# Kernel tuning notes

Hardware: AMD Instinct MI355X
Metric: run time of the kernel (lower is better)

## Reference

```python
import jax, jax.numpy as jnp
import numpy as np

N, NODE_F, EDGE_F = 50000, 192, 64
M = 800000  # directed edges
D = NODE_F + EDGE_F  # inner_dim = 256
OUT = 2048
DEPTH = 3


def setup_inputs() -> dict:
    key = jax.random.key(0)
    ks = jax.random.split(key, 8)
    node_attr = jax.random.normal(ks[0], (N, NODE_F), dtype=jnp.float32)
    edge_attr = jax.random.normal(ks[1], (M, EDGE_F), dtype=jnp.float32)
    edge_src = jax.random.randint(ks[2], (M,), 0, N, dtype=jnp.int32)
    edge_dst = jax.random.randint(ks[3], (M,), 0, N, dtype=jnp.int32)
    # per-depth parameters (original stacks copies along a depth axis)
    W_inner = jnp.stack([jnp.eye(D, dtype=jnp.float32)
                         + 0.01 * jax.random.normal(jax.random.fold_in(ks[4], d), (D, D))
                         for d in range(DEPTH)])                      # [DEPTH, D, D]
    b_inner = jnp.zeros((DEPTH, D), dtype=jnp.float32)
    scale = jnp.sqrt(6.0 / (D + OUT)).astype(jnp.float32)            # glorot_uniform
    W_output = jax.random.uniform(ks[5], (DEPTH + 1, D, OUT), jnp.float32, -scale, scale)
    b_output = jnp.zeros((DEPTH + 1, OUT), dtype=jnp.float32)
    return {"node_attr": node_attr, "edge_attr": edge_attr,
            "edge_src": edge_src, "edge_dst": edge_dst,
            "W_inner": W_inner, "b_inner": b_inner,
            "W_output": W_output, "b_output": b_output}


def _fp_contribution(attr, W_out_d, b_out_d):
    # softmax over fingerprint dim per node, summed over nodes -> [OUT]
    return jax.nn.softmax(attr @ W_out_d + b_out_d, axis=-1).sum(axis=0)


def reference(node_attr, edge_attr, edge_src, edge_dst,
              W_inner, b_inner, W_output, b_output):
    n = node_attr.shape[0]
    # attributes = [nodeAttributes | zeros(edge_feat)]  -> [N, D]
    attr = jnp.concatenate(
        [node_attr, jnp.zeros((n, edge_attr.shape[1]), node_attr.dtype)], axis=1)
    fp = _fp_contribution(attr, W_output[0], b_output[0])
    # per-edge payload: [zeros(node_feat) | edgeAttr]  -> [M, D]
    edge_pad = jnp.concatenate(
        [jnp.zeros((edge_attr.shape[0], node_attr.shape[1]), edge_attr.dtype), edge_attr],
        axis=1)
    for d in range(1, DEPTH + 1):
        # v_i = attr_i + sum_{(ni,ei) in nbrs(i)} (attr_ni + [0|edgeAttr_ei])
        msgs = attr[edge_src] + edge_pad                 # [M, D] gather
        agg = jax.ops.segment_sum(msgs, edge_dst, num_segments=n)
        v = attr + agg
        # activation_inner = 'linear' (identity)
        attr = v @ W_inner[d - 1] + b_inner[d - 1]
        fp = fp + _fp_contribution(attr, W_output[d], b_output[d])
    return fp  # [OUT]
```

## Files before the change

### kernel.cpp

```cpp
#include <hip/hip_runtime.h>
#include <hip/hip_bf16.h>

#define N_NODES 50000
#define N_PAD   50016
#define NODE_F  192
#define EDGE_F  64
#define DIM     256
#define OUT_DIM 2048
#define DEPTH   3
#define M_EDGES 800000

typedef short  bf16x8 __attribute__((ext_vector_type(8)));
typedef float  f32x4  __attribute__((ext_vector_type(4)));

__device__ inline short f2bf(float f) {
    unsigned u = __float_as_uint(f);
    unsigned r = (u + 0x7fffu + ((u >> 16) & 1u)) >> 16;
    return (short)r;
}

__global__ void k_init_attr(const float* __restrict__ node_attr,
                            float* __restrict__ attr,
                            short* __restrict__ attr_bf) {
    int i = blockIdx.x * 256 + threadIdx.x;
    int row = i >> 6, q = i & 63;
    if (row >= N_PAD) return;
    float4 v = make_float4(0.f, 0.f, 0.f, 0.f);
    if (row < N_NODES && q < NODE_F / 4)
        v = ((const float4*)node_attr)[row * (NODE_F / 4) + q];
    if (row < N_NODES) ((float4*)attr)[i] = v;
    short4 s; s.x = f2bf(v.x); s.y = f2bf(v.y); s.z = f2bf(v.z); s.w = f2bf(v.w);
    ((short4*)attr_bf)[i] = s;
}

__global__ void k_degree(const int* __restrict__ dst, int* __restrict__ deg) {
    int e = blockIdx.x * 256 + threadIdx.x;
    if (e < M_EDGES) atomicAdd(&deg[dst[e]], 1);
}

__global__ __launch_bounds__(1024) void k_scan(int* __restrict__ deg,
                                               int* __restrict__ rowptr) {
    __shared__ int part[1024];
    int t = threadIdx.x;
    const int CH = (N_NODES + 1023) / 1024;
    int beg = t * CH, end = min(beg + CH, N_NODES);
    int s = 0;
    for (int i = beg; i < end; i++) s += deg[i];
    part[t] = s;
    __syncthreads();
    for (int off = 1; off < 1024; off <<= 1) {
        int v = (t >= off) ? part[t - off] : 0;
        __syncthreads();
        part[t] += v;
        __syncthreads();
    }
    int run = (t == 0) ? 0 : part[t - 1];
    for (int i = beg; i < end; i++) {
        int d = deg[i];
        rowptr[i] = run;
        deg[i] = run;
        run += d;
    }
    if (t == 1023) rowptr[N_NODES] = run;
}

__global__ void k_fill(const int* __restrict__ dst, const int* __restrict__ src,
                       int* __restrict__ cursor,
                       int* __restrict__ eidx, int* __restrict__ srcs) {
    int e = blockIdx.x * 256 + threadIdx.x;
    if (e < M_EDGES) {
        int p = atomicAdd(&cursor[dst[e]], 1);
        eidx[p] = e;
        srcs[p] = src[e];
    }
}

__global__ __launch_bounds__(256) void k_esum(const float* __restrict__ edge_attr,
                                              const int* __restrict__ rowptr,
                                              const int* __restrict__ eidx,
                                              float* __restrict__ esum) {
    int gid = blockIdx.x * 256 + threadIdx.x;
    int node = gid >> 4, q = gid & 15;
    if (node >= N_NODES) return;
    int beg = rowptr[node], end = rowptr[node + 1];
    float4 acc = make_float4(0.f, 0.f, 0.f, 0.f);
    const float4* E4 = (const float4*)edge_attr;
    for (int i = beg; i < end; i++) {
        int e = eidx[i];
        float4 v = E4[(size_t)e * 16 + q];
        acc.x += v.x; acc.y += v.y; acc.z += v.z; acc.w += v.w;
    }
    ((float4*)esum)[(size_t)node * 16 + q] = acc;
}

__global__ __launch_bounds__(256) void k_gather(const float* __restrict__ attr,
                                                const int* __restrict__ rowptr,
                                                const int* __restrict__ srcs,
                                                const float* __restrict__ esum,
                                                float* __restrict__ agg) {
    int gid = blockIdx.x * 256 + threadIdx.x;
    int node = gid >> 6, q = gid & 63;
    if (node >= N_NODES) return;
    int beg = rowptr[node], end = rowptr[node + 1];
    float4 acc = make_float4(0.f, 0.f, 0.f, 0.f);
    if (q >= NODE_F / 4)
        acc = ((const float4*)esum)[(size_t)node * 16 + (q - NODE_F / 4)];
    const float4* A4 = (const float4*)attr;
    for (int i = beg; i < end; i++) {
        int s = srcs[i];
        float4 v = A4[(size_t)s * 64 + q];
        acc.x += v.x; acc.y += v.y; acc.z += v.z; acc.w += v.w;
    }
    ((float4*)agg)[(size_t)node * 64 + q] = acc;
}

__global__ __launch_bounds__(256) void k_inner(const float* __restrict__ attr,
                                               const float* __restrict__ agg,
                                               const float* __restrict__ W,
                                               const float* __restrict__ b,
                                               float* __restrict__ out,
                                               short* __restrict__ out_bf) {
    __shared__ float4 sV[32][64];
    int tid  = threadIdx.x;
    int row0 = blockIdx.x * 32;

    for (int i = tid; i < 32 * 64; i += 256) {
        int r = i >> 6, q = i & 63;
        int grow = row0 + r;
        float4 v = make_float4(0.f, 0.f, 0.f, 0.f);
        if (grow < N_NODES) {
            float4 a = ((const float4*)attr)[(size_t)grow * 64 + q];
            float4 g = ((const float4*)agg)[(size_t)grow * 64 + q];
            v = make_float4(a.x + g.x, a.y + g.y, a.z + g.z, a.w + g.w);
        }
        sV[r][q] = v;
    }
    __syncthreads();

    int cg = tid & 63;
    int rg = tid >> 6;

    float4 acc[8];
#pragma unroll
    for (int r = 0; r < 8; r++) acc[r] = make_float4(0.f, 0.f, 0.f, 0.f);

    const float4* W4 = (const float4*)W;
    for (int k4 = 0; k4 < 64; k4++) {
        float4 w0 = W4[(size_t)(k4 * 4 + 0) * 64 + cg];
        float4 w1 = W4[(size_t)(k4 * 4 + 1) * 64 + cg];
        float4 w2 = W4[(size_t)(k4 * 4 + 2) * 64 + cg];
        float4 w3 = W4[(size_t)(k4 * 4 + 3) * 64 + cg];
#pragma unroll
        for (int r = 0; r < 8; r++) {
            float4 a = sV[rg * 8 + r][k4];
            acc[r].x += a.x * w0.x + a.y * w1.x + a.z * w2.x + a.w * w3.x;
            acc[r].y += a.x * w0.y + a.y * w1.y + a.z * w2.y + a.w * w3.y;
            acc[r].z += a.x * w0.z + a.y * w1.z + a.z * w2.z + a.w * w3.z;
            acc[r].w += a.x * w0.w + a.y * w1.w + a.z * w2.w + a.w * w3.w;
        }
    }

    float4 bb = ((const float4*)b)[cg];
#pragma unroll
    for (int r = 0; r < 8; r++) {
        int grow = row0 + rg * 8 + r;
        if (grow < N_NODES) {
            float4 o = make_float4(acc[r].x + bb.x, acc[r].y + bb.y,
                                   acc[r].z + bb.z, acc[r].w + bb.w);
            ((float4*)out)[(size_t)grow * 64 + cg] = o;
            short4 s; s.x = f2bf(o.x); s.y = f2bf(o.y); s.z = f2bf(o.z); s.w = f2bf(o.w);
            ((short4*)out_bf)[(size_t)grow * 64 + cg] = s;
        }
    }
}

__global__ void k_wswz(const float* __restrict__ W, short* __restrict__ Wz) {
    int idx = blockIdx.x * 256 + threadIdx.x;
    int lane = idx & 63;
    int T    = (idx >> 6) & 127;
    int ks   = (idx >> 13) & 7;
    int d    = idx >> 16;
    int quad = lane >> 4;
    int m    = lane & 15;
    const float* src = W + ((size_t)(d * 256 + ks * 32 + quad * 8)) * 2048 + T * 16 + m;
    short* dstp = Wz + (size_t)idx * 8;
#pragma unroll
    for (int j = 0; j < 8; j++) dstp[j] = f2bf(src[(size_t)j * 2048]);
}

__global__ __launch_bounds__(1024)
void k_fp_mfma(const short* __restrict__ attr_bf,
               const short* __restrict__ Wz,
               const float* __restrict__ bias,
               float* __restrict__ fp_part) {
    __shared__ float sred[32][17];
    __shared__ float sfinm[32];
    __shared__ float sfinl[32];
    int tid  = threadIdx.x;
    int lane = tid & 63;
    int wave = tid >> 6;
    int quad = lane >> 4;
    int m    = lane & 15;
    int row0 = blockIdx.x * 32;

    f32x4 acc0[8], acc1[8];
#pragma unroll
    for (int t = 0; t < 8; t++) {
        acc0[t] = (f32x4){0.f, 0.f, 0.f, 0.f};
        acc1[t] = (f32x4){0.f, 0.f, 0.f, 0.f};
    }

    const short* a0p = attr_bf + (size_t)(row0 + m) * 256 + quad * 8;
    const short* a1p = a0p + 16 * 256;
    for (int ks = 0; ks < 8; ks++) {
        bf16x8 af0 = *(const bf16x8*)(a0p + ks * 32);
        bf16x8 af1 = *(const bf16x8*)(a1p + ks * 32);
        const bf16x8* bp = (const bf16x8*)Wz + ((size_t)ks * 128 + wave * 8) * 64 + lane;
#pragma unroll
        for (int t = 0; t < 8; t++) {
            bf16x8 bf = bp[t * 64];
            acc0[t] = __builtin_amdgcn_mfma_f32_16x16x32_bf16(af0, bf, acc0[t], 0, 0, 0);
            acc1[t] = __builtin_amdgcn_mfma_f32_16x16x32_bf16(af1, bf, acc1[t], 0, 0, 0);
        }
    }

#pragma unroll
    for (int t = 0; t < 8; t++) {
        float bb = bias[(wave * 8 + t) * 16 + m];
        acc0[t][0] += bb; acc0[t][1] += bb; acc0[t][2] += bb; acc0[t][3] += bb;
        acc1[t][0] += bb; acc1[t][1] += bb; acc1[t][2] += bb; acc1[t][3] += bb;
    }

    float mx0[4], mx1[4];
#pragma unroll
    for (int r = 0; r < 4; r++) {
        float v0 = acc0[0][r], v1 = acc1[0][r];
#pragma unroll
        for (int t = 1; t < 8; t++) { v0 = fmaxf(v0, acc0[t][r]); v1 = fmaxf(v1, acc1[t][r]); }
        mx0[r] = v0; mx1[r] = v1;
    }
#pragma unroll
    for (int off = 1; off < 16; off <<= 1)
#pragma unroll
        for (int r = 0; r < 4; r++) {
            mx0[r] = fmaxf(mx0[r], __shfl_xor(mx0[r], off));
            mx1[r] = fmaxf(mx1[r], __shfl_xor(mx1[r], off));
        }
    if (m == 0)
#pragma unroll
        for (int r = 0; r < 4; r++) {
            sred[quad * 4 + r][wave]      = mx0[r];
            sred[16 + quad * 4 + r][wave] = mx1[r];
        }
    __syncthreads();
    if (tid < 32) {
        float v = sred[tid][0];
#pragma unroll
        for (int w = 1; w < 16; w++) v = fmaxf(v, sred[tid][w]);
        sfinm[tid] = v;
    }
    __syncthreads();
#pragma unroll
    for (int r = 0; r < 4; r++) { mx0[r] = sfinm[quad * 4 + r]; mx1[r] = sfinm[16 + quad * 4 + r]; }

    float ls0[4] = {0.f, 0.f, 0.f, 0.f}, ls1[4] = {0.f, 0.f, 0.f, 0.f};
#pragma unroll
    for (int t = 0; t < 8; t++) {
#pragma unroll
        for (int r = 0; r < 4; r++) {
            float e0 = __expf(acc0[t][r] - mx0[r]);
            float e1 = __expf(acc1[t][r] - mx1[r]);
            acc0[t][r] = e0; acc1[t][r] = e1;
            ls0[r] += e0; ls1[r] += e1;
        }
    }
#pragma unroll
    for (int off = 1; off < 16; off <<= 1)
#pragma unroll
        for (int r = 0; r < 4; r++) {
            ls0[r] += __shfl_xor(ls0[r], off);
            ls1[r] += __shfl_xor(ls1[r], off);
        }
    if (m == 0)
#pragma unroll
        for (int r = 0; r < 4; r++) {
            sred[quad * 4 + r][wave]      = ls0[r];
            sred[16 + quad * 4 + r][wave] = ls1[r];
        }
    __syncthreads();
    if (tid < 32) {
        float v = 0.f;
#pragma unroll
        for (int w = 0; w < 16; w++) v += sred[tid][w];
        sfinl[tid] = v;
    }
    __syncthreads();

    float rinv0[4], rinv1[4];
#pragma unroll
    for (int r = 0; r < 4; r++) {
        int ra = quad * 4 + r, rb = 16 + quad * 4 + r;
        rinv0[r] = (row0 + ra < N_NODES) ? 1.0f / sfinl[ra] : 0.0f;
        rinv1[r] = (row0 + rb < N_NODES) ? 1.0f / sfinl[rb] : 0.0f;
    }

    float* dst = fp_part + (size_t)(blockIdx.x & 63) * OUT_DIM;
#pragma unroll
    for (int t = 0; t < 8; t++) {
        float cs = acc0[t][0] * rinv0[0] + acc0[t][1] * rinv0[1]
                 + acc0[t][2] * rinv0[2] + acc0[t][3] * rinv0[3]
                 + acc1[t][0] * rinv1[0] + acc1[t][1] * rinv1[1]
                 + acc1[t][2] * rinv1[2] + acc1[t][3] * rinv1[3];
        cs += __shfl_xor(cs, 16);
        cs += __shfl_xor(cs, 32);
        if (quad == 0)
            atomicAdd(&dst[(wave * 8 + t) * 16 + m], cs);
    }
}

__global__ void k_fp_reduce(const float* __restrict__ part, float* __restrict__ fp) {
    int c = blockIdx.x * 256 + threadIdx.x;
    float s = 0.f;
#pragma unroll
    for (int r = 0; r < 64; r++) s += part[(size_t)r * OUT_DIM + c];
    fp[c] = s;
}

extern "C" void kernel_launch(void* const* d_in, const int* in_sizes, int n_in,
                              void* d_out, int out_size, void* d_ws, size_t ws_size,
                              hipStream_t stream) {
    const float* node_attr = (const float*)d_in[0];
    const float* edge_attr = (const float*)d_in[1];
    const int*   edge_src  = (const int*)d_in[2];
    const int*   edge_dst  = (const int*)d_in[3];
    const float* W_inner   = (const float*)d_in[4];
    const float* b_inner   = (const float*)d_in[5];
    const float* W_output  = (const float*)d_in[6];
    const float* b_output  = (const float*)d_in[7];

    float* fp      = (float*)d_out;
    float* attr    = (float*)d_ws;
    float* agg     = attr + (size_t)N_NODES * DIM;
    float* fp_part = agg + (size_t)N_NODES * DIM;
    short* Wz      = (short*)(fp_part + 64 * OUT_DIM);
    int*   deg     = (int*)(Wz + (size_t)4 * 65536 * 8);
    int*   rowptr  = deg + N_NODES;
    int*   eidx    = rowptr + N_NODES + 1;
    int*   srcs    = eidx + M_EDGES;
    float* esum    = (float*)(srcs + M_EDGES);
    short* attr_bf = (short*)(esum + (size_t)N_NODES * EDGE_F);

    hipMemsetAsync(fp_part, 0, 64 * OUT_DIM * sizeof(float), stream);
    hipMemsetAsync(deg, 0, N_NODES * sizeof(int), stream);

    k_init_attr<<<(N_PAD * 64 + 255) / 256, 256, 0, stream>>>(node_attr, attr, attr_bf);

    k_degree<<<(M_EDGES + 255) / 256, 256, 0, stream>>>(edge_dst, deg);
    k_scan<<<1, 1024, 0, stream>>>(deg, rowptr);
    k_fill<<<(M_EDGES + 255) / 256, 256, 0, stream>>>(edge_dst, edge_src, deg, eidx, srcs);
    k_esum<<<(N_NODES * 16 + 255) / 256, 256, 0, stream>>>(edge_attr, rowptr, eidx, esum);

    k_wswz<<<1024, 256, 0, stream>>>(W_output, Wz);

    k_fp_mfma<<<N_PAD / 32, 1024, 0, stream>>>(attr_bf, Wz, b_output, fp_part);

    for (int d = 1; d <= DEPTH; d++) {
        k_gather<<<(N_NODES * 64 + 255) / 256, 256, 0, stream>>>(
            attr, rowptr, srcs, esum, agg);
        k_inner<<<(N_NODES + 31) / 32, 256, 0, stream>>>(
            attr, agg, W_inner + (size_t)(d - 1) * DIM * DIM,
            b_inner + (size_t)(d - 1) * DIM, attr, attr_bf);
        k_fp_mfma<<<N_PAD / 32, 1024, 0, stream>>>(
            attr_bf, Wz + (size_t)d * 65536 * 8,
            b_output + (size_t)d * OUT_DIM, fp_part);
    }
    k_fp_reduce<<<OUT_DIM / 256, 256, 0, stream>>>(fp_part, fp);
}
```

Measured before the change: 1.867 ms.

## Stage fingerprint GEMM operands through LDS with double-buffered async global loads

The fingerprint MFMA kernel now loads the attribute tile into swizzled LDS and streams the output-weight tiles into a double-buffered LDS region using direct global-to-LDS loads. Explicit waitcnt and barrier calls overlap the next tile's fetch with the MFMAs, and the MFMAs run at raised wave priority. Previously each wave read the weights straight from global memory with no prefetch. The weight swizzle kernel is relaid out to match the staging order, and the partial-sum buffer is halved from 64 to 32 slices, which adds more atomic contention per slice. The extra LDS use may limit occupancy, and the hand-written wait counts must match the number of loads in flight.

```diff
diff --git a/kernel.cpp b/kernel.cpp
--- a/kernel.cpp
+++ b/kernel.cpp
@@ -18,6 +18,12 @@
     unsigned r = (u + 0x7fffu + ((u >> 16) & 1u)) >> 16;
     return (short)r;
 }
+
+#define GLDS16(g, l) __builtin_amdgcn_global_load_lds(                        \
+    (const __attribute__((address_space(1))) void*)(g),                       \
+    (__attribute__((address_space(3))) void*)(l), 16, 0, 0)
+
+#define MEMFENCE() asm volatile("" ::: "memory")
 
 __global__ void k_init_attr(const float* __restrict__ node_attr,
                             float* __restrict__ attr,
@@ -183,9 +189,11 @@
     int quad = lane >> 4;
     int m    = lane & 15;
     const float* src = W + ((size_t)(d * 256 + ks * 32 + quad * 8)) * 2048 + T * 16 + m;
-    short* dstp = Wz + (size_t)idx * 8;
-#pragma unroll
-    for (int j = 0; j < 8; j++) dstp[j] = f2bf(src[(size_t)j * 2048]);
+    int w = T >> 3, h = (T >> 2) & 1, j = T & 3;
+    size_t n = ((((size_t)(ks * 2 + h)) * 16 + w) * 4 + j) * 64 + lane;
+    short* dstp = Wz + ((size_t)d * 65536 + n) * 8;
+#pragma unroll
+    for (int jj = 0; jj < 8; jj++) dstp[jj] = f2bf(src[(size_t)jj * 2048]);
 }
 
 __global__ __launch_bounds__(1024)
@@ -193,6 +201,8 @@
                const short* __restrict__ Wz,
                const float* __restrict__ bias,
                float* __restrict__ fp_part) {
+    __shared__ __align__(16) short A_lds[32 * 256];
+    __shared__ __align__(16) short B_lds[2][4096 * 8];
     __shared__ float sred[32][17];
     __shared__ float sfinm[32];
     __shared__ float sfinl[32];
@@ -202,6 +212,28 @@
     int quad = lane >> 4;
     int m    = lane & 15;
     int row0 = blockIdx.x * 32;
+    int sw   = (m & 7) << 4;
+
+    {
+        int r   = tid >> 5;
+        int c16 = tid & 31;
+        const char* gsrc = (const char*)attr_bf
+            + (size_t)(row0 + r) * 512 + (size_t)((c16 * 16) ^ ((r & 7) << 4));
+        char* ldst = (char*)A_lds + (size_t)wave * 1024;
+        GLDS16(gsrc, ldst);
+    }
+    MEMFENCE();
+    auto stage_unit = [&](int uu, int b) {
+        const char* gb = (const char*)Wz + (size_t)uu * 65536 + (size_t)tid * 16;
+        char* lb = (char*)(&B_lds[b][0]) + wave * 1024;
+#pragma unroll
+        for (int p = 0; p < 4; p++)
+            GLDS16(gb + p * 16384, lb + p * 16384);
+    };
+    stage_unit(0, 0);
+    MEMFENCE();
+    stage_unit(1, 1);
+    MEMFENCE();
 
     f32x4 acc0[8], acc1[8];
 #pragma unroll
@@ -210,18 +242,38 @@
         acc1[t] = (f32x4){0.f, 0.f, 0.f, 0.f};
     }
 
-    const short* a0p = attr_bf + (size_t)(row0 + m) * 256 + quad * 8;
-    const short* a1p = a0p + 16 * 256;
-    for (int ks = 0; ks < 8; ks++) {
-        bf16x8 af0 = *(const bf16x8*)(a0p + ks * 32);
-        bf16x8 af1 = *(const bf16x8*)(a1p + ks * 32);
-        const bf16x8* bp = (const bf16x8*)Wz + ((size_t)ks * 128 + wave * 8) * 64 + lane;
-#pragma unroll
-        for (int t = 0; t < 8; t++) {
-            bf16x8 bf = bp[t * 64];
-            acc0[t] = __builtin_amdgcn_mfma_f32_16x16x32_bf16(af0, bf, acc0[t], 0, 0, 0);
-            acc1[t] = __builtin_amdgcn_mfma_f32_16x16x32_bf16(af1, bf, acc1[t], 0, 0, 0);
-        }
+    bf16x8 af0, af1;
+#pragma unroll
+    for (int u = 0; u < 16; u++) {
+        if (u == 0 || u == 15) asm volatile("s_waitcnt vmcnt(0)" ::: "memory");
+        else                   asm volatile("s_waitcnt vmcnt(4)" ::: "memory");
+        __builtin_amdgcn_s_barrier();
+        if ((u & 1) == 0) {
+            int co = (quad * 16 + (u >> 1) * 64) ^ sw;
+            af0 = *(const bf16x8*)((const char*)A_lds + m * 512 + co);
+            af1 = *(const bf16x8*)((const char*)A_lds + (m + 16) * 512 + co);
+        }
+        const char* Bb = (const char*)(&B_lds[u & 1][0])
+                       + ((size_t)(wave * 4) * 64 + lane) * 16;
+        bf16x8 b0 = *(const bf16x8*)(Bb);
+        bf16x8 b1 = *(const bf16x8*)(Bb + 1024);
+        bf16x8 b2 = *(const bf16x8*)(Bb + 2048);
+        bf16x8 b3 = *(const bf16x8*)(Bb + 3072);
+        asm volatile("s_waitcnt lgkmcnt(0)" ::: "memory");
+        __builtin_amdgcn_s_barrier();
+        if (u < 14) stage_unit(u + 2, u & 1);
+        MEMFENCE();
+        int t0 = (u & 1) * 4;
+        __builtin_amdgcn_s_setprio(1);
+        acc0[t0 + 0] = __builtin_amdgcn_mfma_f32_16x16x32_bf16(af0, b0, acc0[t0 + 0], 0, 0, 0);
+        acc1[t0 + 0] = __builtin_amdgcn_mfma_f32_16x16x32_bf16(af1, b0, acc1[t0 + 0], 0, 0, 0);
+        acc0[t0 + 1] = __builtin_amdgcn_mfma_f32_16x16x32_bf16(af0, b1, acc0[t0 + 1], 0, 0, 0);
+        acc1[t0 + 1] = __builtin_amdgcn_mfma_f32_16x16x32_bf16(af1, b1, acc1[t0 + 1], 0, 0, 0);
+        acc0[t0 + 2] = __builtin_amdgcn_mfma_f32_16x16x32_bf16(af0, b2, acc0[t0 + 2], 0, 0, 0);
+        acc1[t0 + 2] = __builtin_amdgcn_mfma_f32_16x16x32_bf16(af1, b2, acc1[t0 + 2], 0, 0, 0);
+        acc0[t0 + 3] = __builtin_amdgcn_mfma_f32_16x16x32_bf16(af0, b3, acc0[t0 + 3], 0, 0, 0);
+        acc1[t0 + 3] = __builtin_amdgcn_mfma_f32_16x16x32_bf16(af1, b3, acc1[t0 + 3], 0, 0, 0);
+        __builtin_amdgcn_s_setprio(0);
     }
 
 #pragma unroll
@@ -304,7 +356,7 @@
         rinv1[r] = (row0 + rb < N_NODES) ? 1.0f / sfinl[rb] : 0.0f;
     }
 
-    float* dst = fp_part + (size_t)(blockIdx.x & 63) * OUT_DIM;
+    float* dst = fp_part + (size_t)(blockIdx.x & 31) * OUT_DIM;
 #pragma unroll
     for (int t = 0; t < 8; t++) {
         float cs = acc0[t][0] * rinv0[0] + acc0[t][1] * rinv0[1]
@@ -322,7 +374,7 @@
     int c = blockIdx.x * 256 + threadIdx.x;
     float s = 0.f;
 #pragma unroll
-    for (int r = 0; r < 64; r++) s += part[(size_t)r * OUT_DIM + c];
+    for (int r = 0; r < 32; r++) s += part[(size_t)r * OUT_DIM + c];
     fp[c] = s;
 }
 
@@ -342,15 +394,15 @@
     float* attr    = (float*)d_ws;
     float* agg     = attr + (size_t)N_NODES * DIM;
     float* fp_part = agg + (size_t)N_NODES * DIM;
-    short* Wz      = (short*)(fp_part + 64 * OUT_DIM);
+    short* Wz      = (short*)(fp_part + 32 * OUT_DIM);
     int*   deg     = (int*)(Wz + (size_t)4 * 65536 * 8);
     int*   rowptr  = deg + N_NODES;
-    int*   eidx    = rowptr + N_NODES + 1;
+    int*   eidx    = rowptr + N_NODES + 4;
     int*   srcs    = eidx + M_EDGES;
     float* esum    = (float*)(srcs + M_EDGES);
     short* attr_bf = (short*)(esum + (size_t)N_NODES * EDGE_F);
 
-    hipMemsetAsync(fp_part, 0, 64 * OUT_DIM * sizeof(float), stream);
+    hipMemsetAsync(fp_part, 0, 32 * OUT_DIM * sizeof(float), stream);
     hipMemsetAsync(deg, 0, N_NODES * sizeof(int), stream);
 
     k_init_attr<<<(N_PAD * 64 + 255) / 256, 256, 0, stream>>>(node_attr, attr, attr_bf);
```

Measured after the change: 1.768 ms. 1.06x faster.
